# Kernel optimization log

Measured on AMD Instinct MI355X. Metric: run time of the kernel, lower is better.

## Reference

```python
import jax, jax.numpy as jnp
import numpy as np

DT_MIN, DT_MAX = 1e-3, 1e-1
LN_EPS = 1e-5


def layernorm(x, w, b):
    mu = jnp.mean(x, axis=-1, keepdims=True)
    var = jnp.mean(jnp.square(x - mu), axis=-1, keepdims=True)
    return (x - mu) * jax.lax.rsqrt(var + LN_EPS) * w + b


def _scan(Lam_bar, Bu, reverse=False):
    # Lam_bar: (P,) complex64; Bu: (B, L, P) complex64
    A = jnp.broadcast_to(Lam_bar, Bu.shape)

    def binop(e_i, e_j):
        a_i, b_i = e_i
        a_j, b_j = e_j
        return a_j * a_i, a_j * b_i + b_j

    _, xs = jax.lax.associative_scan(binop, (A, Bu), axis=1, reverse=reverse)
    return xs  # (B, L, P)


def s5_ssm(u, Lambda_re, Lambda_im, log_step, B_re, B_im, C_re, C_im, D):
    # u: (B, L, H) real. Diagonal S5 with ZOH discretization, bidirectional.
    step = jnp.exp(log_step)                          # (P,)
    Lam = (Lambda_re + 1j * Lambda_im).astype(jnp.complex64)
    Lam_bar = jnp.exp(Lam * step)                     # (P,)
    Bmat = (B_re + 1j * B_im).astype(jnp.complex64)   # (P, H)
    B_bar = ((Lam_bar - 1.0) / Lam)[:, None] * Bmat   # (P, H)
    Bu = jnp.einsum('blh,ph->blp', u.astype(jnp.complex64), B_bar)  # (B,L,P)
    xs_f = _scan(Lam_bar, Bu, reverse=False)
    xs_b = _scan(Lam_bar, Bu, reverse=True)
    xs = jnp.concatenate([xs_f, xs_b], axis=-1)       # (B, L, 2P)
    C = (C_re + 1j * C_im).astype(jnp.complex64)      # (H, 2P)
    ys = 2.0 * jnp.einsum('hp,blp->blh', C, xs).real  # conj-symmetric output
    return ys + D * u


def gelu(x):
    return jax.nn.gelu(x, approximate=False)  # torch default (erf) gelu


def s5_block(x, ln1_w, ln1_b, ln2_w, ln2_b, Lambda_re, Lambda_im, log_step,
             B_re, B_im, C_re, C_im, D, ff_enc_w, ff_dec_w):
    # attention-style half: pre-LN + S5 + gelu + residual (residual = normed input)
    fx = layernorm(x, ln1_w, ln1_b)
    res = fx
    x = gelu(s5_ssm(fx, Lambda_re, Lambda_im, log_step, B_re, B_im, C_re, C_im, D)) + res
    # FFN half: pre-LN + GEGLU + residual (residual = normed input)
    fx = layernorm(x, ln2_w, ln2_b)
    res = fx
    h = fx @ ff_enc_w.T                               # (B, L, 2*dim)
    a, g = jnp.split(h, 2, axis=-1)
    x = (a * gelu(g)) @ ff_dec_w.T + res
    return x


def setup_inputs() -> dict:
    B, L, D_IN, DIM, P = 4, 4096, 512, 1024, 512
    key = jax.random.key(0)
    ks = jax.random.split(key, 16)
    inp = {}
    inp['x'] = jax.random.normal(ks[0], (B, L, D_IN), dtype=jnp.float32)
    inp['W_in'] = jax.random.normal(ks[1], (DIM, D_IN), jnp.float32) / np.sqrt(D_IN)
    inp['W_out'] = jax.random.normal(ks[2], (D_IN, DIM), jnp.float32) / np.sqrt(DIM)
    inp['ln1_w'] = jnp.ones((DIM,), jnp.float32)
    inp['ln1_b'] = jnp.zeros((DIM,), jnp.float32)
    inp['ln2_w'] = jnp.ones((DIM,), jnp.float32)
    inp['ln2_b'] = jnp.zeros((DIM,), jnp.float32)
    inp['Lambda_re'] = -0.5 * jnp.exp(jax.random.normal(ks[3], (P,), jnp.float32))
    inp['Lambda_im'] = jnp.pi * jax.random.normal(ks[4], (P,), jnp.float32)
    inp['log_step'] = jax.random.uniform(ks[5], (P,), jnp.float32,
                                         minval=np.log(DT_MIN), maxval=np.log(DT_MAX))
    inp['B_re'] = jax.random.normal(ks[6], (P, DIM), jnp.float32) / np.sqrt(DIM)
    inp['B_im'] = jax.random.normal(ks[7], (P, DIM), jnp.float32) / np.sqrt(DIM)
    inp['C_re'] = jax.random.normal(ks[8], (DIM, 2 * P), jnp.float32) / np.sqrt(2 * P)
    inp['C_im'] = jax.random.normal(ks[9], (DIM, 2 * P), jnp.float32) / np.sqrt(2 * P)
    inp['D'] = jax.random.normal(ks[10], (DIM,), jnp.float32)
    inp['ff_enc_w'] = jax.random.normal(ks[11], (2 * DIM, DIM), jnp.float32) / np.sqrt(DIM)
    inp['ff_dec_w'] = jax.random.normal(ks[12], (DIM, DIM), jnp.float32) / np.sqrt(DIM)
    return inp


def reference(x, W_in, W_out, ln1_w, ln1_b, ln2_w, ln2_b, Lambda_re, Lambda_im,
              log_step, B_re, B_im, C_re, C_im, D, ff_enc_w, ff_dec_w):
    h = x @ W_in.T                                    # (B, L, dim)
    h = s5_block(h, ln1_w, ln1_b, ln2_w, ln2_b, Lambda_re, Lambda_im, log_step,
                 B_re, B_im, C_re, C_im, D, ff_enc_w, ff_dec_w)
    return h @ W_out.T                                # (B, L, d_input)
```

## Files before the change

### kernel.cpp

```cpp
#include <hip/hip_runtime.h>
#include <cstdint>

typedef __bf16 bf16;
typedef __bf16 bf16x2 __attribute__((ext_vector_type(2)));
typedef __bf16 bf16x4 __attribute__((ext_vector_type(4)));
typedef __bf16 bf16x8 __attribute__((ext_vector_type(8)));
typedef float f32x4 __attribute__((ext_vector_type(4)));

#define MROWS 16384
#define DIMH 1024
#define PDIM 512
#define LSEQ 4096
#define CL 16
#define NC (LSEQ / CL)

typedef const __attribute__((address_space(1))) unsigned int* gas_t;
typedef __attribute__((address_space(3))) unsigned int* las_t;

__device__ __forceinline__ float gelu_f(float x) {
  return 0.5f * x * (1.0f + erff(x * 0.70710678118654752f));
}

__global__ __launch_bounds__(256) void k_mega(
    const float* __restrict__ x, const float* __restrict__ W_in,
    const float* __restrict__ W_out, const float* __restrict__ ffe,
    const float* __restrict__ ffd, const float* __restrict__ Lre,
    const float* __restrict__ Lim, const float* __restrict__ lstep,
    const float* __restrict__ Bre, const float* __restrict__ Bim,
    const float* __restrict__ Cre, const float* __restrict__ Cim,
    bf16* __restrict__ xb, bf16* __restrict__ winb, bf16* __restrict__ woutb,
    bf16* __restrict__ ffeb, bf16* __restrict__ ffdb, bf16* __restrict__ bcat,
    bf16* __restrict__ cc, float2* __restrict__ lamb) {
  const int bid = blockIdx.x;
  const int tid = threadIdx.x;
  auto cvt4 = [&](const float* src, bf16* dst, int i4) {
    const float4 v = *(const float4*)(src + i4);
    bf16x4 o = { (bf16)v.x, (bf16)v.y, (bf16)v.z, (bf16)v.w };
    *(bf16x4*)(dst + i4) = o;
  };
  if (bid < 8192) {
    cvt4(x, xb, bid * 1024 + tid * 4);
  } else if (bid < 8704) {
    cvt4(W_in, winb, (bid - 8192) * 1024 + tid * 4);
  } else if (bid < 9216) {
    cvt4(W_out, woutb, (bid - 8704) * 1024 + tid * 4);
  } else if (bid < 11264) {
    cvt4(ffe, ffeb, (bid - 9216) * 1024 + tid * 4);
  } else if (bid < 12288) {
    cvt4(ffd, ffdb, (bid - 11264) * 1024 + tid * 4);
  } else if (bid < 12800) {
    const int i4 = (bid - 12288) * 1024 + tid * 4;
    const int p = i4 >> 10;
    const float lre = Lre[p], lim = Lim[p];
    const float st = expf(lstep[p]);
    const float er = expf(lre * st);
    const float lbr = er * cosf(lim * st);
    const float lbi = er * sinf(lim * st);
    const float ar = lbr - 1.0f, ai = lbi;
    const float d = lre * lre + lim * lim;
    const float cx = (ar * lre + ai * lim) / d;
    const float cy = (ai * lre - ar * lim) / d;
    const float4 br = *(const float4*)(Bre + i4);
    const float4 bi = *(const float4*)(Bim + i4);
    bf16x4 o1 = { (bf16)(cx * br.x - cy * bi.x), (bf16)(cx * br.y - cy * bi.y),
                  (bf16)(cx * br.z - cy * bi.z), (bf16)(cx * br.w - cy * bi.w) };
    bf16x4 o2 = { (bf16)(cx * bi.x + cy * br.x), (bf16)(cx * bi.y + cy * br.y),
                  (bf16)(cx * bi.z + cy * br.z), (bf16)(cx * bi.w + cy * br.w) };
    *(bf16x4*)(bcat + i4) = o1;
    *(bf16x4*)(bcat + i4 + PDIM * DIMH) = o2;
  } else if (bid < 14848) {
    const int i4 = (bid - 12800) * 1024 + tid * 4;
    const int n = i4 >> 11, k0 = i4 & 2047;
    const float* src;
    float sgn;
    int kk;
    if (k0 < 512)       { src = Cre + n * 1024;       sgn =  2.0f; kk = k0; }
    else if (k0 < 1024) { src = Cim + n * 1024;       sgn = -2.0f; kk = k0 - 512; }
    else if (k0 < 1536) { src = Cre + n * 1024 + 512; sgn =  2.0f; kk = k0 - 1024; }
    else                { src = Cim + n * 1024 + 512; sgn = -2.0f; kk = k0 - 1536; }
    const float4 v = *(const float4*)(src + kk);
    bf16x4 o = { (bf16)(sgn * v.x), (bf16)(sgn * v.y), (bf16)(sgn * v.z), (bf16)(sgn * v.w) };
    *(bf16x4*)(cc + i4) = o;
  } else {
    const int p = (bid - 14848) * 256 + tid;
    if (p < PDIM) {
      const float lre = Lre[p], lim = Lim[p];
      const float st = expf(lstep[p]);
      const float er = expf(lre * st);
      lamb[p] = make_float2(er * cosf(lim * st), er * sinf(lim * st));
    }
  }
}

#define VMCNT4 asm volatile("s_waitcnt vmcnt(4)" ::: "memory")
#define VMCNT0 asm volatile("s_waitcnt vmcnt(0)" ::: "memory")
#define LGKM0  asm volatile("s_waitcnt lgkmcnt(0)" ::: "memory")
#define SCHED0 __builtin_amdgcn_sched_barrier(0)
#define BAR    __builtin_amdgcn_s_barrier()

template <int EPI>
__global__ __launch_bounds__(256, 3) void k_gemm(const bf16* __restrict__ A,
                                                 const bf16* __restrict__ W,
                                                 float* __restrict__ Cf,
                                                 bf16* __restrict__ Cb,
                                                 const bf16* __restrict__ auxb,
                                                 int K, int N, int nbnl) {
  extern __shared__ char lds[];
  const int q = (int)gridDim.x >> 3;
  const int s = ((int)blockIdx.x & 7) * q + ((int)blockIdx.x >> 3);
  const int bm = s >> nbnl;
  const int bn = s & ((1 << nbnl) - 1);
  const int tid = threadIdx.x;
  const int lane = tid & 63;
  const int wave = tid >> 6;
  const int wr = wave >> 1;
  const int wc = wave & 1;

  const size_t arow0 = (size_t)bm * 128;
  const size_t wrow0 = (size_t)bn * 128;
  const int srow = tid >> 2;
  const int schunk = (tid & 3) ^ ((tid >> 3) & 3);
  const int wbase = wave << 10;

  f32x4 acc[4][4];
#pragma unroll
  for (int i = 0; i < 4; ++i)
#pragma unroll
    for (int j = 0; j < 4; ++j) acc[i][j] = (f32x4){0.f, 0.f, 0.f, 0.f};

  auto stage = [&](int buf, int ui) {
    const int kcol = ui * 32 + schunk * 8;
    char* ba = lds + buf * 16384;
    __builtin_amdgcn_global_load_lds(
        (gas_t)(A + (arow0 + srow) * (size_t)K + kcol), (las_t)(ba + wbase), 16, 0, 0);
    __builtin_amdgcn_global_load_lds(
        (gas_t)(A + (arow0 + 64 + srow) * (size_t)K + kcol), (las_t)(ba + 4096 + wbase), 16, 0, 0);
    char* bb = ba + 8192;
    __builtin_amdgcn_global_load_lds(
        (gas_t)(W + (wrow0 + srow) * (size_t)K + kcol), (las_t)(bb + wbase), 16, 0, 0);
    __builtin_amdgcn_global_load_lds(
        (gas_t)(W + (wrow0 + 64 + srow) * (size_t)K + kcol), (las_t)(bb + 4096 + wbase), 16, 0, 0);
  };

  auto ldA = [&](int buf, bf16x8* af) {
#pragma unroll
    for (int m = 0; m < 4; ++m) {
      const int row = wr * 64 + m * 16 + (lane & 15);
      const int pc = (lane >> 4) ^ ((row >> 1) & 3);
      af[m] = *(const bf16x8*)(lds + buf * 16384 + row * 64 + pc * 16);
    }
  };
  auto ldB = [&](int buf, bf16x8* bf) {
#pragma unroll
    for (int n = 0; n < 4; ++n) {
      const int row = wc * 64 + n * 16 + (lane & 15);
      const int pc = (lane >> 4) ^ ((row >> 1) & 3);
      bf[n] = *(const bf16x8*)(lds + buf * 16384 + 8192 + row * 64 + pc * 16);
    }
  };

  bf16x8 afr[4], bfr[4];

  stage(0, 0);
  stage(1, 1);
  VMCNT4;
  BAR;

  const int NU = K >> 5;
  int buf = 0, sbuf = 2;
  for (int u = 0; u < NU; ++u) {
    ldB(buf, bfr);
    ldA(buf, afr);
    if (u + 2 < NU) stage(sbuf, u + 2);
    LGKM0; SCHED0;
    __builtin_amdgcn_s_setprio(1);
#pragma unroll
    for (int m = 0; m < 4; ++m)
#pragma unroll
      for (int n = 0; n < 4; ++n)
        acc[m][n] = __builtin_amdgcn_mfma_f32_16x16x32_bf16(afr[m], bfr[n], acc[m][n], 0, 0, 0);
    __builtin_amdgcn_s_setprio(0);
    SCHED0;
    if (u + 2 < NU) { VMCNT4; }
    else if (u + 1 < NU) { VMCNT0; }
    BAR;
    buf = (buf == 2) ? 0 : buf + 1;
    sbuf = (sbuf == 2) ? 0 : sbuf + 1;
  }

  const int n0 = (int)wrow0 + wc * 64 + (lane & 15);
  const size_t m0 = arow0 + wr * 64 + ((lane >> 4) << 2);
#pragma unroll
  for (int mi = 0; mi < 4; ++mi)
#pragma unroll
    for (int n = 0; n < 4; ++n) {
      const size_t mb = m0 + mi * 16;
      const int nn = n0 + n * 16;
#pragma unroll
      for (int r = 0; r < 4; ++r) {
        const size_t idx = (mb + r) * (size_t)N + nn;
        const float v = acc[mi][n][r];
        if constexpr (EPI == 0) {
          Cf[idx] = v;
        } else if constexpr (EPI == 1) {
          Cb[idx] = (bf16)((float)auxb[idx] * gelu_f(v));
        } else if constexpr (EPI == 2) {
          Cb[idx] = (bf16)(v + (float)auxb[idx]);
        } else {
          Cb[idx] = (bf16)v;
        }
      }
    }
}

#define PHASE2(slot, kh, mh, LOADB, STAGE_STMT, WAIT_STMT)                     \
  {                                                                            \
    if (LOADB) ldB(slot, kh, bfr);                                             \
    ldA(slot, kh, mh, afr);                                                    \
    STAGE_STMT;                                                                \
    SCHED0;                                                                    \
    BAR;                                                                       \
    LGKM0;                                                                     \
    SCHED0;                                                                    \
    __builtin_amdgcn_s_setprio(1);                                             \
    _Pragma("unroll")                                                          \
    for (int m = 0; m < 4; ++m)                                                \
      _Pragma("unroll")                                                        \
      for (int n = 0; n < 4; ++n)                                              \
        acc[(mh) * 4 + m][n] = __builtin_amdgcn_mfma_f32_16x16x32_bf16(        \
            afr[m], bfr[n], acc[(mh) * 4 + m][n], 0, 0, 0);                    \
    __builtin_amdgcn_s_setprio(0);                                             \
    SCHED0;                                                                    \
    WAIT_STMT;                                                                 \
    BAR;                                                                       \
  }

template <int EPI>
__global__ __launch_bounds__(512, 2) void k_gemm2(const bf16* __restrict__ A,
                                                  const bf16* __restrict__ W,
                                                  float* __restrict__ Cf,
                                                  bf16* __restrict__ Cb,
                                                  const bf16* __restrict__ auxb,
                                                  int K, int N, int nbnl) {
  extern __shared__ char lds[];
  const int q = (int)gridDim.x >> 3;
  const int s = ((int)blockIdx.x & 7) * q + ((int)blockIdx.x >> 3);
  const int bm = s >> nbnl;
  const int bn = s & ((1 << nbnl) - 1);
  const int tid = threadIdx.x;
  const int lane = tid & 63;
  const int wave = tid >> 6;
  const int wr = wave >> 2;
  const int wc = wave & 3;

  const size_t arow0 = (size_t)bm * 256;
  const size_t wrow0 = (size_t)bn * 256;
  const int srow = tid >> 2;
  const int schunk = (tid & 3) ^ ((tid >> 3) & 3);
  const int wbase = wave << 10;

  f32x4 acc[8][4];
#pragma unroll
  for (int i = 0; i < 8; ++i)
#pragma unroll
    for (int j = 0; j < 4; ++j) acc[i][j] = (f32x4){0.f, 0.f, 0.f, 0.f};

  auto stage = [&](int slot, int kh, int kt) {
    const int kcol = kt * 64 + kh * 32 + schunk * 8;
    {
      char* base = lds + slot * 32768 + kh * 16384;
      __builtin_amdgcn_global_load_lds(
          (gas_t)(A + (arow0 + srow) * (size_t)K + kcol), (las_t)(base + wbase), 16, 0, 0);
      __builtin_amdgcn_global_load_lds(
          (gas_t)(A + (arow0 + 128 + srow) * (size_t)K + kcol), (las_t)(base + 8192 + wbase), 16, 0, 0);
    }
    {
      char* base = lds + 65536 + slot * 32768 + kh * 16384;
      __builtin_amdgcn_global_load_lds(
          (gas_t)(W + (wrow0 + srow) * (size_t)K + kcol), (las_t)(base + wbase), 16, 0, 0);
      __builtin_amdgcn_global_load_lds(
          (gas_t)(W + (wrow0 + 128 + srow) * (size_t)K + kcol), (las_t)(base + 8192 + wbase), 16, 0, 0);
    }
  };

  auto ldA = [&](int slot, int kh, int mh, bf16x8* af) {
#pragma unroll
    for (int m = 0; m < 4; ++m) {
      const int row = wr * 128 + mh * 64 + m * 16 + (lane & 15);
      const int pc = (lane >> 4) ^ ((row >> 1) & 3);
      af[m] = *(const bf16x8*)(lds + slot * 32768 + kh * 16384 + row * 64 + pc * 16);
    }
  };
  auto ldB = [&](int slot, int kh, bf16x8* bf) {
#pragma unroll
    for (int n = 0; n < 4; ++n) {
      const int row = wc * 64 + n * 16 + (lane & 15);
      const int pc = (lane >> 4) ^ ((row >> 1) & 3);
      bf[n] = *(const bf16x8*)(lds + 65536 + slot * 32768 + kh * 16384 + row * 64 + pc * 16);
    }
  };

  bf16x8 afr[4], bfr[4];

  stage(0, 0, 0);
  stage(0, 1, 0);
  stage(1, 0, 1);
  VMCNT4;
  BAR;

  const int NT = K >> 7;
  for (int t = 0; t < NT; ++t) {
    const int nl = (t + 1 < NT);
    PHASE2(0, 0, 0, 1, stage(1, 1, 2 * t + 1), (void)0);
    PHASE2(0, 0, 1, 0, (void)0, (void)0);
    PHASE2(0, 1, 0, 1, if (nl) stage(0, 0, 2 * t + 2), (void)0);
    if (nl) { PHASE2(0, 1, 1, 0, (void)0, VMCNT4); }
    else    { PHASE2(0, 1, 1, 0, (void)0, VMCNT0); }
    PHASE2(1, 0, 0, 1, if (nl) stage(0, 1, 2 * t + 2), (void)0);
    PHASE2(1, 0, 1, 0, (void)0, (void)0);
    PHASE2(1, 1, 0, 1, if (nl) stage(1, 0, 2 * t + 3), (void)0);
    if (nl) { PHASE2(1, 1, 1, 0, (void)0, VMCNT4); }
    else    { PHASE2(1, 1, 1, 0, (void)0, (void)0); }
  }

  const int n0 = (int)wrow0 + wc * 64 + (lane & 15);
  const size_t m0 = arow0 + wr * 128 + ((lane >> 4) << 2);
#pragma unroll
  for (int mi = 0; mi < 8; ++mi)
#pragma unroll
    for (int n = 0; n < 4; ++n) {
      const size_t mb = m0 + mi * 16;
      const int nn = n0 + n * 16;
#pragma unroll
      for (int r = 0; r < 4; ++r) {
        const size_t idx = (mb + r) * (size_t)N + nn;
        const float v = acc[mi][n][r];
        if constexpr (EPI == 0) {
          Cf[idx] = v;
        } else {
          Cb[idx] = (bf16)v;
        }
      }
    }
}

__global__ __launch_bounds__(256) void k_ln(const bf16* __restrict__ X,
                                            const float* __restrict__ w,
                                            const float* __restrict__ bb,
                                            bf16* __restrict__ Yb) {
  const int m = blockIdx.x;
  const int tid = threadIdx.x;
  const bf16x4 v4 = *(const bf16x4*)(X + (size_t)m * DIMH + tid * 4);
  const float v0 = (float)v4[0], v1 = (float)v4[1], v2 = (float)v4[2], v3 = (float)v4[3];
  float s = v0 + v1 + v2 + v3;
  float s2 = v0 * v0 + v1 * v1 + v2 * v2 + v3 * v3;
#pragma unroll
  for (int off = 32; off > 0; off >>= 1) { s += __shfl_down(s, off); s2 += __shfl_down(s2, off); }
  __shared__ float rs[4], rq[4];
  if ((tid & 63) == 0) { rs[tid >> 6] = s; rq[tid >> 6] = s2; }
  __syncthreads();
  s = rs[0] + rs[1] + rs[2] + rs[3];
  s2 = rq[0] + rq[1] + rq[2] + rq[3];
  const float mu = s * (1.0f / DIMH);
  const float inv = rsqrtf(s2 * (1.0f / DIMH) - mu * mu + 1e-5f);
  const float4 wv = ((const float4*)w)[tid];
  const float4 bv = ((const float4*)bb)[tid];
  bf16x4 ob = { (bf16)((v0 - mu) * inv * wv.x + bv.x), (bf16)((v1 - mu) * inv * wv.y + bv.y),
                (bf16)((v2 - mu) * inv * wv.z + bv.z), (bf16)((v3 - mu) * inv * wv.w + bv.w) };
  *(bf16x4*)(Yb + (size_t)m * DIMH + tid * 4) = ob;
}

__global__ __launch_bounds__(256) void k_ln2e(const bf16* __restrict__ YS,
                                              bf16* FXE,
                                              const float* __restrict__ Dv,
                                              const float* __restrict__ w,
                                              const float* __restrict__ bb) {
  const int m = blockIdx.x;
  const int tid = threadIdx.x;
  const bf16x4 ys4 = *(const bf16x4*)(YS + (size_t)m * DIMH + tid * 4);
  const bf16x4 fx4 = *(const bf16x4*)(FXE + (size_t)m * DIMH + tid * 4);
  const float4 dv = ((const float4*)Dv)[tid];
  const float f0 = (float)fx4[0], f1 = (float)fx4[1], f2 = (float)fx4[2], f3 = (float)fx4[3];
  const float t0 = gelu_f((float)ys4[0] + dv.x * f0) + f0;
  const float t1 = gelu_f((float)ys4[1] + dv.y * f1) + f1;
  const float t2 = gelu_f((float)ys4[2] + dv.z * f2) + f2;
  const float t3 = gelu_f((float)ys4[3] + dv.w * f3) + f3;
  float s = t0 + t1 + t2 + t3;
  float s2 = t0 * t0 + t1 * t1 + t2 * t2 + t3 * t3;
#pragma unroll
  for (int off = 32; off > 0; off >>= 1) { s += __shfl_down(s, off); s2 += __shfl_down(s2, off); }
  __shared__ float rs[4], rq[4];
  if ((tid & 63) == 0) { rs[tid >> 6] = s; rq[tid >> 6] = s2; }
  __syncthreads();
  s = rs[0] + rs[1] + rs[2] + rs[3];
  s2 = rq[0] + rq[1] + rq[2] + rq[3];
  const float mu = s * (1.0f / DIMH);
  const float inv = rsqrtf(s2 * (1.0f / DIMH) - mu * mu + 1e-5f);
  const float4 wv = ((const float4*)w)[tid];
  const float4 bv = ((const float4*)bb)[tid];
  bf16x4 ob = { (bf16)((t0 - mu) * inv * wv.x + bv.x), (bf16)((t1 - mu) * inv * wv.y + bv.y),
                (bf16)((t2 - mu) * inv * wv.z + bv.z), (bf16)((t3 - mu) * inv * wv.w + bv.w) };
  *(bf16x4*)(FXE + (size_t)m * DIMH + tid * 4) = ob;
}

__global__ __launch_bounds__(256) void k_scanA(const bf16* __restrict__ Bu,
                                               const float2* __restrict__ lamb,
                                               float2* __restrict__ carry) {
  const int bc = blockIdx.x;
  const int b = bc >> 8, c = bc & (NC - 1);
  const int t = threadIdx.x;
  const size_t rbase = ((size_t)b * LSEQ + (size_t)c * CL) * DIMH;
  float2 re[CL], im[CL];
#pragma unroll
  for (int i = 0; i < CL; ++i) {
    const bf16x2 r2 = *(const bf16x2*)(Bu + rbase + (size_t)i * DIMH + 2 * t);
    const bf16x2 i2 = *(const bf16x2*)(Bu + rbase + (size_t)i * DIMH + PDIM + 2 * t);
    re[i] = make_float2((float)r2[0], (float)r2[1]);
    im[i] = make_float2((float)i2[0], (float)i2[1]);
  }
  const float2 l0 = lamb[2 * t];
  const float2 l1 = lamb[2 * t + 1];
  const size_t cb = ((size_t)bc * 2) * PDIM;
  {
    float s0r = 0.f, s0i = 0.f, s1r = 0.f, s1i = 0.f;
#pragma unroll
    for (int i = 0; i < CL; ++i) {
      float nr = l0.x * s0r - l0.y * s0i + re[i].x;
      float ni = l0.x * s0i + l0.y * s0r + im[i].x;
      s0r = nr; s0i = ni;
      nr = l1.x * s1r - l1.y * s1i + re[i].y;
      ni = l1.x * s1i + l1.y * s1r + im[i].y;
      s1r = nr; s1i = ni;
    }
    carry[cb + 2 * t]     = make_float2(s0r, s0i);
    carry[cb + 2 * t + 1] = make_float2(s1r, s1i);
  }
  {
    float s0r = 0.f, s0i = 0.f, s1r = 0.f, s1i = 0.f;
#pragma unroll
    for (int i = CL - 1; i >= 0; --i) {
      float nr = l0.x * s0r - l0.y * s0i + re[i].x;
      float ni = l0.x * s0i + l0.y * s0r + im[i].x;
      s0r = nr; s0i = ni;
      nr = l1.x * s1r - l1.y * s1i + re[i].y;
      ni = l1.x * s1i + l1.y * s1r + im[i].y;
      s1r = nr; s1i = ni;
    }
    carry[cb + PDIM + 2 * t]     = make_float2(s0r, s0i);
    carry[cb + PDIM + 2 * t + 1] = make_float2(s1r, s1i);
  }
}

__global__ __launch_bounds__(256) void k_scanB(const float2* __restrict__ carry,
                                               const float2* __restrict__ lamb,
                                               float2* __restrict__ seed) {
  const int b = blockIdx.x;
  const int t = threadIdx.x;
  const float2 l0 = lamb[2 * t], l1 = lamb[2 * t + 1];
  float L0r = l0.x, L0i = l0.y, L1r = l1.x, L1i = l1.y;
#pragma unroll
  for (int q = 0; q < 4; ++q) {
    float tr = L0r * L0r - L0i * L0i; L0i = 2.f * L0r * L0i; L0r = tr;
    tr = L1r * L1r - L1i * L1i; L1i = 2.f * L1r * L1i; L1r = tr;
  }
  float S0r = 0.f, S0i = 0.f, S1r = 0.f, S1i = 0.f;
  for (int c = 0; c < NC; ++c) {
    const size_t base = (((size_t)b * NC + c) * 2) * PDIM;
    const float2 c0 = carry[base + 2 * t];
    const float2 c1 = carry[base + 2 * t + 1];
    seed[base + 2 * t]     = make_float2(S0r, S0i);
    seed[base + 2 * t + 1] = make_float2(S1r, S1i);
    float nr = L0r * S0r - L0i * S0i + c0.x;
    float ni = L0r * S0i + L0i * S0r + c0.y;
    S0r = nr; S0i = ni;
    nr = L1r * S1r - L1i * S1i + c1.x;
    ni = L1r * S1i + L1i * S1r + c1.y;
    S1r = nr; S1i = ni;
  }
  S0r = 0.f; S0i = 0.f; S1r = 0.f; S1i = 0.f;
  for (int c = NC - 1; c >= 0; --c) {
    const size_t base = (((size_t)b * NC + c) * 2) * PDIM + PDIM;
    const float2 c0 = carry[base + 2 * t];
    const float2 c1 = carry[base + 2 * t + 1];
    seed[base + 2 * t]     = make_float2(S0r, S0i);
    seed[base + 2 * t + 1] = make_float2(S1r, S1i);
    float nr = L0r * S0r - L0i * S0i + c0.x;
    float ni = L0r * S0i + L0i * S0r + c0.y;
    S0r = nr; S0i = ni;
    nr = L1r * S1r - L1i * S1i + c1.x;
    ni = L1r * S1i + L1i * S1r + c1.y;
    S1r = nr; S1i = ni;
  }
}

__global__ __launch_bounds__(256) void k_scanC(const bf16* __restrict__ Bu,
                                               const float2* __restrict__ lamb,
                                               const float2* __restrict__ seed,
                                               bf16* __restrict__ xs) {
  const int bc = blockIdx.x;
  const int b = bc >> 8, c = bc & (NC - 1);
  const int t = threadIdx.x;
  const size_t rbase = ((size_t)b * LSEQ + (size_t)c * CL) * DIMH;
  float2 re[CL], im[CL];
#pragma unroll
  for (int i = 0; i < CL; ++i) {
    const bf16x2 r2 = *(const bf16x2*)(Bu + rbase + (size_t)i * DIMH + 2 * t);
    const bf16x2 i2 = *(const bf16x2*)(Bu + rbase + (size_t)i * DIMH + PDIM + 2 * t);
    re[i] = make_float2((float)r2[0], (float)r2[1]);
    im[i] = make_float2((float)i2[0], (float)i2[1]);
  }
  const float2 l0 = lamb[2 * t];
  const float2 l1 = lamb[2 * t + 1];
  const size_t sb = ((size_t)bc * 2) * PDIM;
  const size_t obase = ((size_t)b * LSEQ + (size_t)c * CL) * 2048;
  {
    const float2 s0 = seed[sb + 2 * t];
    const float2 s1 = seed[sb + 2 * t + 1];
    float s0r = s0.x, s0i = s0.y, s1r = s1.x, s1i = s1.y;
#pragma unroll
    for (int i = 0; i < CL; ++i) {
      float nr = l0.x * s0r - l0.y * s0i + re[i].x;
      float ni = l0.x * s0i + l0.y * s0r + im[i].x;
      s0r = nr; s0i = ni;
      nr = l1.x * s1r - l1.y * s1i + re[i].y;
      ni = l1.x * s1i + l1.y * s1r + im[i].y;
      s1r = nr; s1i = ni;
      bf16x2 wr2 = { (bf16)s0r, (bf16)s1r };
      bf16x2 wi2 = { (bf16)s0i, (bf16)s1i };
      *(bf16x2*)(xs + obase + (size_t)i * 2048 + 2 * t) = wr2;
      *(bf16x2*)(xs + obase + (size_t)i * 2048 + PDIM + 2 * t) = wi2;
    }
  }
  {
    const float2 s0 = seed[sb + PDIM + 2 * t];
    const float2 s1 = seed[sb + PDIM + 2 * t + 1];
    float s0r = s0.x, s0i = s0.y, s1r = s1.x, s1i = s1.y;
#pragma unroll
    for (int i = CL - 1; i >= 0; --i) {
      float nr = l0.x * s0r - l0.y * s0i + re[i].x;
      float ni = l0.x * s0i + l0.y * s0r + im[i].x;
      s0r = nr; s0i = ni;
      nr = l1.x * s1r - l1.y * s1i + re[i].y;
      ni = l1.x * s1i + l1.y * s1r + im[i].y;
      s1r = nr; s1i = ni;
      bf16x2 wr2 = { (bf16)s0r, (bf16)s1r };
      bf16x2 wi2 = { (bf16)s0i, (bf16)s1i };
      *(bf16x2*)(xs + obase + (size_t)i * 2048 + 1024 + 2 * t) = wr2;
      *(bf16x2*)(xs + obase + (size_t)i * 2048 + 1536 + 2 * t) = wi2;
    }
  }
}

extern "C" void kernel_launch(void* const* d_in, const int* in_sizes, int n_in,
                              void* d_out, int out_size, void* d_ws, size_t ws_size,
                              hipStream_t stream) {
  const float* x    = (const float*)d_in[0];
  const float* W_in = (const float*)d_in[1];
  const float* W_out= (const float*)d_in[2];
  const float* ln1w = (const float*)d_in[3];
  const float* ln1b = (const float*)d_in[4];
  const float* ln2w = (const float*)d_in[5];
  const float* ln2b = (const float*)d_in[6];
  const float* Lre  = (const float*)d_in[7];
  const float* Lim  = (const float*)d_in[8];
  const float* lstep= (const float*)d_in[9];
  const float* Bre  = (const float*)d_in[10];
  const float* Bim  = (const float*)d_in[11];
  const float* Cre  = (const float*)d_in[12];
  const float* Cim  = (const float*)d_in[13];
  const float* Dv   = (const float*)d_in[14];
  const float* ffe  = (const float*)d_in[15];
  const float* ffd  = (const float*)d_in[16];
  float* out = (float*)d_out;
  char* ws = (char*)d_ws;

  bf16* winb   = (bf16*)(ws);
  bf16* woutb  = (bf16*)(ws + (1u << 20));
  bf16* bcat   = (bf16*)(ws + (2u << 20));
  bf16* ccomb  = (bf16*)(ws + (4u << 20));
  bf16* ffeb   = (bf16*)(ws + (8u << 20));
  bf16* ffdb   = (bf16*)(ws + (12u << 20));
  float2* lamb = (float2*)(ws + (14u << 20));
  bf16* E      = (bf16*)(ws + (16u << 20));
  bf16* hb     = (bf16*)(ws + (48u << 20));
  bf16* Bub    = (bf16*)(ws + (48u << 20));
  bf16* ysb    = (bf16*)(ws + (48u << 20));
  bf16* x3b    = (bf16*)(ws + (48u << 20));
  bf16* xsb    = (bf16*)(ws + (80u << 20));
  bf16* a_b    = (bf16*)(ws + (80u << 20));
  bf16* G      = (bf16*)(ws + (112u << 20));
  float2* carry = (float2*)(ws + (144u << 20));
  float2* seed  = (float2*)(ws + (152u << 20));

  static bool attr_done = false;
  if (!attr_done) {
    hipFuncSetAttribute((const void*)&k_gemm<0>, hipFuncAttributeMaxDynamicSharedMemorySize, 49152);
    hipFuncSetAttribute((const void*)&k_gemm<1>, hipFuncAttributeMaxDynamicSharedMemorySize, 49152);
    hipFuncSetAttribute((const void*)&k_gemm<2>, hipFuncAttributeMaxDynamicSharedMemorySize, 49152);
    hipFuncSetAttribute((const void*)&k_gemm<3>, hipFuncAttributeMaxDynamicSharedMemorySize, 49152);
    hipFuncSetAttribute((const void*)&k_gemm2<3>, hipFuncAttributeMaxDynamicSharedMemorySize, 131072);
    attr_done = true;
  }

  k_mega<<<14850, 256, 0, stream>>>(x, W_in, W_out, ffe, ffd, Lre, Lim, lstep,
                                    Bre, Bim, Cre, Cim,
                                    E, winb, woutb, ffeb, ffdb, bcat, ccomb, lamb);

  k_gemm<3><<<1024, 256, 49152, stream>>>(E, winb, nullptr, hb, nullptr, 512, 1024, 3);
  k_ln<<<16384, 256, 0, stream>>>(hb, ln1w, ln1b, E);
  k_gemm<3><<<1024, 256, 49152, stream>>>(E, bcat, nullptr, Bub, nullptr, 1024, 1024, 3);
  k_scanA<<<4 * NC, 256, 0, stream>>>(Bub, lamb, carry);
  k_scanB<<<4, 256, 0, stream>>>(carry, lamb, seed);
  k_scanC<<<4 * NC, 256, 0, stream>>>(Bub, lamb, seed, xsb);
  k_gemm2<3><<<256, 512, 131072, stream>>>(xsb, ccomb, nullptr, ysb, nullptr, 2048, 1024, 2);
  k_ln2e<<<16384, 256, 0, stream>>>(ysb, E, Dv, ln2w, ln2b);
  k_gemm<3><<<1024, 256, 49152, stream>>>(E, ffeb, nullptr, a_b, nullptr, 1024, 1024, 3);
  k_gemm<1><<<1024, 256, 49152, stream>>>(E, ffeb + (size_t)1024 * 1024, nullptr, G, a_b, 1024, 1024, 3);
  k_gemm<2><<<1024, 256, 49152, stream>>>(G, ffdb, nullptr, x3b, E, 1024, 1024, 3);
  k_gemm<0><<<512, 256, 49152, stream>>>(x3b, woutb, out, nullptr, nullptr, 1024, 512, 2);
}
```

Baseline: 449.5 us.

## Restructure k_gemm2 pipeline into triple-buffered single-barrier k-steps

Rewrites the 256x256 GEMM used for the C projection. The old version used a two-slot, half-k phased schedule with two barriers per phase. The new one runs a 3-stage ring of 32-wide k-slices with one barrier per step and all 8x4 MFMAs issued per step. LDS use drops from 128KB to 96KB and launch bounds change to 1 block per CU. The aim is to cut barrier and sync overhead; the risk is less latency hiding from the lower occupancy and from more A fragments held in registers.

Measured after the change: 448.1 us. About the same (-0.3%).

```diff
diff --git a/kernel.cpp b/kernel.cpp
--- a/kernel.cpp
+++ b/kernel.cpp
@@ -213,34 +213,11 @@
     }
 }
 
-#define PHASE2(slot, kh, mh, LOADB, STAGE_STMT, WAIT_STMT)                     \
-  {                                                                            \
-    if (LOADB) ldB(slot, kh, bfr);                                             \
-    ldA(slot, kh, mh, afr);                                                    \
-    STAGE_STMT;                                                                \
-    SCHED0;                                                                    \
-    BAR;                                                                       \
-    LGKM0;                                                                     \
-    SCHED0;                                                                    \
-    __builtin_amdgcn_s_setprio(1);                                             \
-    _Pragma("unroll")                                                          \
-    for (int m = 0; m < 4; ++m)                                                \
-      _Pragma("unroll")                                                        \
-      for (int n = 0; n < 4; ++n)                                              \
-        acc[(mh) * 4 + m][n] = __builtin_amdgcn_mfma_f32_16x16x32_bf16(        \
-            afr[m], bfr[n], acc[(mh) * 4 + m][n], 0, 0, 0);                    \
-    __builtin_amdgcn_s_setprio(0);                                             \
-    SCHED0;                                                                    \
-    WAIT_STMT;                                                                 \
-    BAR;                                                                       \
-  }
-
 template <int EPI>
-__global__ __launch_bounds__(512, 2) void k_gemm2(const bf16* __restrict__ A,
+__global__ __launch_bounds__(512, 1) void k_gemm2(const bf16* __restrict__ A,
                                                   const bf16* __restrict__ W,
                                                   float* __restrict__ Cf,
                                                   bf16* __restrict__ Cb,
-                                                  const bf16* __restrict__ auxb,
                                                   int K, int N, int nbnl) {
   extern __shared__ char lds[];
   const int q = (int)gridDim.x >> 3;
@@ -265,62 +242,64 @@
 #pragma unroll
     for (int j = 0; j < 4; ++j) acc[i][j] = (f32x4){0.f, 0.f, 0.f, 0.f};
 
-  auto stage = [&](int slot, int kh, int kt) {
-    const int kcol = kt * 64 + kh * 32 + schunk * 8;
-    {
-      char* base = lds + slot * 32768 + kh * 16384;
-      __builtin_amdgcn_global_load_lds(
-          (gas_t)(A + (arow0 + srow) * (size_t)K + kcol), (las_t)(base + wbase), 16, 0, 0);
-      __builtin_amdgcn_global_load_lds(
-          (gas_t)(A + (arow0 + 128 + srow) * (size_t)K + kcol), (las_t)(base + 8192 + wbase), 16, 0, 0);
-    }
-    {
-      char* base = lds + 65536 + slot * 32768 + kh * 16384;
-      __builtin_amdgcn_global_load_lds(
-          (gas_t)(W + (wrow0 + srow) * (size_t)K + kcol), (las_t)(base + wbase), 16, 0, 0);
-      __builtin_amdgcn_global_load_lds(
-          (gas_t)(W + (wrow0 + 128 + srow) * (size_t)K + kcol), (las_t)(base + 8192 + wbase), 16, 0, 0);
-    }
+  auto stage = [&](int buf, int ui) {
+    const int kcol = ui * 32 + schunk * 8;
+    char* ba = lds + buf * 32768;
+    __builtin_amdgcn_global_load_lds(
+        (gas_t)(A + (arow0 + srow) * (size_t)K + kcol), (las_t)(ba + wbase), 16, 0, 0);
+    __builtin_amdgcn_global_load_lds(
+        (gas_t)(A + (arow0 + 128 + srow) * (size_t)K + kcol), (las_t)(ba + 8192 + wbase), 16, 0, 0);
+    char* bb = ba + 16384;
+    __builtin_amdgcn_global_load_lds(
+        (gas_t)(W + (wrow0 + srow) * (size_t)K + kcol), (las_t)(bb + wbase), 16, 0, 0);
+    __builtin_amdgcn_global_load_lds(
+        (gas_t)(W + (wrow0 + 128 + srow) * (size_t)K + kcol), (las_t)(bb + 8192 + wbase), 16, 0, 0);
   };
 
-  auto ldA = [&](int slot, int kh, int mh, bf16x8* af) {
-#pragma unroll
-    for (int m = 0; m < 4; ++m) {
-      const int row = wr * 128 + mh * 64 + m * 16 + (lane & 15);
+  auto ldA = [&](int buf, bf16x8* af) {
+#pragma unroll
+    for (int m = 0; m < 8; ++m) {
+      const int row = wr * 128 + m * 16 + (lane & 15);
       const int pc = (lane >> 4) ^ ((row >> 1) & 3);
-      af[m] = *(const bf16x8*)(lds + slot * 32768 + kh * 16384 + row * 64 + pc * 16);
+      af[m] = *(const bf16x8*)(lds + buf * 32768 + row * 64 + pc * 16);
     }
   };
-  auto ldB = [&](int slot, int kh, bf16x8* bf) {
+  auto ldB = [&](int buf, bf16x8* bf) {
 #pragma unroll
     for (int n = 0; n < 4; ++n) {
       const int row = wc * 64 + n * 16 + (lane & 15);
       const int pc = (lane >> 4) ^ ((row >> 1) & 3);
-      bf[n] = *(const bf16x8*)(lds + 65536 + slot * 32768 + kh * 16384 + row * 64 + pc * 16);
+      bf[n] = *(const bf16x8*)(lds + buf * 32768 + 16384 + row * 64 + pc * 16);
     }
   };
 
-  bf16x8 afr[4], bfr[4];
-
-  stage(0, 0, 0);
-  stage(0, 1, 0);
-  stage(1, 0, 1);
+  bf16x8 afr[8], bfr[4];
+
+  stage(0, 0);
+  stage(1, 1);
   VMCNT4;
   BAR;
 
-  const int NT = K >> 7;
-  for (int t = 0; t < NT; ++t) {
-    const int nl = (t + 1 < NT);
-    PHASE2(0, 0, 0, 1, stage(1, 1, 2 * t + 1), (void)0);
-    PHASE2(0, 0, 1, 0, (void)0, (void)0);
-    PHASE2(0, 1, 0, 1, if (nl) stage(0, 0, 2 * t + 2), (void)0);
-    if (nl) { PHASE2(0, 1, 1, 0, (void)0, VMCNT4); }
-    else    { PHASE2(0, 1, 1, 0, (void)0, VMCNT0); }
-    PHASE2(1, 0, 0, 1, if (nl) stage(0, 1, 2 * t + 2), (void)0);
-    PHASE2(1, 0, 1, 0, (void)0, (void)0);
-    PHASE2(1, 1, 0, 1, if (nl) stage(1, 0, 2 * t + 3), (void)0);
-    if (nl) { PHASE2(1, 1, 1, 0, (void)0, VMCNT4); }
-    else    { PHASE2(1, 1, 1, 0, (void)0, (void)0); }
+  const int NU = K >> 5;
+  int buf = 0, sbuf = 2;
+  for (int u = 0; u < NU; ++u) {
+    ldB(buf, bfr);
+    ldA(buf, afr);
+    if (u + 2 < NU) stage(sbuf, u + 2);
+    LGKM0; SCHED0;
+    __builtin_amdgcn_s_setprio(1);
+#pragma unroll
+    for (int m = 0; m < 8; ++m)
+#pragma unroll
+      for (int n = 0; n < 4; ++n)
+        acc[m][n] = __builtin_amdgcn_mfma_f32_16x16x32_bf16(afr[m], bfr[n], acc[m][n], 0, 0, 0);
+    __builtin_amdgcn_s_setprio(0);
+    SCHED0;
+    if (u + 2 < NU) { VMCNT4; }
+    else if (u + 1 < NU) { VMCNT0; }
+    BAR;
+    buf = (buf == 2) ? 0 : buf + 1;
+    sbuf = (sbuf == 2) ? 0 : sbuf + 1;
   }
 
   const int n0 = (int)wrow0 + wc * 64 + (lane & 15);
@@ -594,11 +573,11 @@
 
   static bool attr_done = false;
   if (!attr_done) {
-    hipFuncSetAttribute((const void*)&k_gemm<0>, hipFuncAttributeMaxDynamicSharedMemorySize, 49152);
-    hipFuncSetAttribute((const void*)&k_gemm<1>, hipFuncAttributeMaxDynamicSharedMemorySize, 49152);
-    hipFuncSetAttribute((const void*)&k_gemm<2>, hipFuncAttributeMaxDynamicSharedMemorySize, 49152);
-    hipFuncSetAttribute((const void*)&k_gemm<3>, hipFuncAttributeMaxDynamicSharedMemorySize, 49152);
-    hipFuncSetAttribute((const void*)&k_gemm2<3>, hipFuncAttributeMaxDynamicSharedMemorySize, 131072);
+    (void)hipFuncSetAttribute((const void*)&k_gemm<0>, hipFuncAttributeMaxDynamicSharedMemorySize, 49152);
+    (void)hipFuncSetAttribute((const void*)&k_gemm<1>, hipFuncAttributeMaxDynamicSharedMemorySize, 49152);
+    (void)hipFuncSetAttribute((const void*)&k_gemm<2>, hipFuncAttributeMaxDynamicSharedMemorySize, 49152);
+    (void)hipFuncSetAttribute((const void*)&k_gemm<3>, hipFuncAttributeMaxDynamicSharedMemorySize, 49152);
+    (void)hipFuncSetAttribute((const void*)&k_gemm2<3>, hipFuncAttributeMaxDynamicSharedMemorySize, 98304);
     attr_done = true;
   }
 
@@ -612,7 +591,7 @@
   k_scanA<<<4 * NC, 256, 0, stream>>>(Bub, lamb, carry);
   k_scanB<<<4, 256, 0, stream>>>(carry, lamb, seed);
   k_scanC<<<4 * NC, 256, 0, stream>>>(Bub, lamb, seed, xsb);
-  k_gemm2<3><<<256, 512, 131072, stream>>>(xsb, ccomb, nullptr, ysb, nullptr, 2048, 1024, 2);
+  k_gemm2<3><<<256, 512, 98304, stream>>>(xsb, ccomb, nullptr, ysb, 2048, 1024, 2);
   k_ln2e<<<16384, 256, 0, stream>>>(ysb, E, Dv, ln2w, ln2b);
   k_gemm<3><<<1024, 256, 49152, stream>>>(E, ffeb, nullptr, a_b, nullptr, 1024, 1024, 3);
   k_gemm<1><<<1024, 256, 49152, stream>>>(E, ffeb + (size_t)1024 * 1024, nullptr, G, a_b, 1024, 1024, 3);
```
